# Performance work log

Measured on AMD Instinct MI355X. Metric: run time of the kernel, lower is better.

Reference implementation:

```python
import jax, jax.numpy as jnp
import numpy as np

TOP_K = 4
NORM_TOPK_PROB = True


def setup_inputs() -> dict:
    key = jax.random.key(0)
    kx, kg, k1, k3, k2 = jax.random.split(key, 5)
    B, S, H, I, E = 1, 2048, 1024, 512, 16
    scale = 0.02
    return {
        "hidden_states": jax.random.normal(kx, (B, S, H), jnp.float32),
        "gate_w": jax.random.normal(kg, (E, H), jnp.float32) * scale,   # router Linear weight [E,H]
        "w1": jax.random.normal(k1, (E, I, H), jnp.float32) * scale,    # intermediateDense per expert
        "w3": jax.random.normal(k3, (E, I, H), jnp.float32) * scale,    # intermediateDense2 per expert
        "w2": jax.random.normal(k2, (E, H, I), jnp.float32) * scale,    # outputDense per expert
    }


def reference(hidden_states, gate_w, w1, w3, w2):
    B, S, H = hidden_states.shape
    x = hidden_states.reshape(-1, H)                    # [T,H]
    T = x.shape[0]
    E = gate_w.shape[0]

    # Router: softmax in fp32, top-k, optional renorm (norm_topk_prob=True)
    router_logits = x @ gate_w.T                        # [T,E]
    probs = jax.nn.softmax(router_logits.astype(jnp.float32), axis=-1)
    routing_weights, selected = jax.lax.top_k(probs, TOP_K)   # [T,K], [T,K]
    if NORM_TOPK_PROB:
        routing_weights = routing_weights / routing_weights.sum(-1, keepdims=True)
    routing_weights = routing_weights.astype(x.dtype)

    # Dense per-token expert-weight matrix: zero for unselected experts, so
    # the combine below computes exactly the torch gather->FFN->index_add math.
    w = jnp.zeros((T, E), x.dtype).at[jnp.arange(T)[:, None], selected].add(routing_weights)

    # Gated SiLU FFN for every expert, combined with routing weights.
    h1 = jnp.einsum('th,eih->tei', x, w1)               # [T,E,I]
    h3 = jnp.einsum('th,eih->tei', x, w3)               # [T,E,I]
    act = jax.nn.silu(h1) * h3                          # [T,E,I]
    out = jnp.einsum('tei,ehi,te->th', act, w2, w)      # [T,H]
    return out.reshape(B, S, H)
```

## Files before the change

### kernel.cpp

```cpp
#include <hip/hip_runtime.h>
#include <hip/hip_bf16.h>

#define T 2048
#define H 1024
#define IDIM 512
#define E 16
#define TOPK 4
#define NPAIR (T * TOPK)

typedef short bf16x8 __attribute__((ext_vector_type(8)));
typedef float f32x4 __attribute__((ext_vector_type(4)));
typedef unsigned short u16x8 __attribute__((ext_vector_type(8)));

static __device__ __forceinline__ unsigned short f2bf(float f) {
    union { float f; unsigned int u; } v; v.f = f;
    unsigned int r = (v.u + 0x7FFFu + ((v.u >> 16) & 1u)) >> 16;
    return (unsigned short)r;
}
static __device__ __forceinline__ float bf2f(unsigned short s) {
    union { unsigned int u; float f; } v; v.u = ((unsigned int)s) << 16;
    return v.f;
}

static __device__ __forceinline__ void async_ld16(const unsigned short* g, unsigned short* l) {
    __builtin_amdgcn_global_load_lds((const __attribute__((address_space(1))) void*)g,
                                     (__attribute__((address_space(3))) void*)l, 16, 0, 0);
}

__global__ __launch_bounds__(256) void router_kernel(
    const float* __restrict__ x, const float* __restrict__ gw,
    int* __restrict__ topk_idx, float* __restrict__ topk_w,
    unsigned short* __restrict__ xb)
{
    int tok = blockIdx.x * 4 + (threadIdx.x >> 6);
    int lane = threadIdx.x & 63;
    if (tok >= T) return;
    const float4* xt4 = (const float4*)(x + (size_t)tok * H);
    float4 xr[4];
#pragma unroll
    for (int j = 0; j < 4; ++j) xr[j] = xt4[lane + j * 64];
    ushort4* xbt = (ushort4*)(xb + (size_t)tok * H);
#pragma unroll
    for (int j = 0; j < 4; ++j) {
        ushort4 o;
        o.x = f2bf(xr[j].x); o.y = f2bf(xr[j].y);
        o.z = f2bf(xr[j].z); o.w = f2bf(xr[j].w);
        xbt[lane + j * 64] = o;
    }
    float logits[E];
#pragma unroll
    for (int e = 0; e < E; ++e) {
        const float4* ge4 = (const float4*)(gw + (size_t)e * H);
        float acc = 0.f;
#pragma unroll
        for (int j = 0; j < 4; ++j) {
            float4 g = ge4[lane + j * 64];
            acc += xr[j].x * g.x + xr[j].y * g.y + xr[j].z * g.z + xr[j].w * g.w;
        }
#pragma unroll
        for (int off = 32; off; off >>= 1) acc += __shfl_xor(acc, off, 64);
        logits[e] = acc;
    }
    if (lane == 0) {
        float m = logits[0];
#pragma unroll
        for (int e = 1; e < E; ++e) m = fmaxf(m, logits[e]);
        float p[E];
#pragma unroll
        for (int e = 0; e < E; ++e) p[e] = __expf(logits[e] - m);
        int sel[TOPK]; float wv[TOPK]; float tot = 0.f;
#pragma unroll
        for (int k = 0; k < TOPK; ++k) {
            int best = 0; float bv = -1.f;
#pragma unroll
            for (int e = 0; e < E; ++e) { if (p[e] > bv) { bv = p[e]; best = e; } }
            sel[k] = best; wv[k] = bv; tot += bv; p[best] = -2.f;
        }
#pragma unroll
        for (int k = 0; k < TOPK; ++k) {
            topk_idx[tok * TOPK + k] = sel[k];
            topk_w[tok * TOPK + k] = wv[k] / tot;
        }
    }
}

__global__ __launch_bounds__(256) void cvtrb_kernel(
    const float* __restrict__ w1, const float* __restrict__ w3, const float* __restrict__ w2,
    unsigned short* __restrict__ d1, unsigned short* __restrict__ d3, unsigned short* __restrict__ d2,
    const int* __restrict__ topk_idx, int* __restrict__ offsets,
    int* __restrict__ pair_token, int* __restrict__ inv_pos)
{
    int tid = threadIdx.x;
    if (blockIdx.x == 0) {
        __shared__ int h[E];
        __shared__ int cur[E];
        if (tid < E) h[tid] = 0;
        __syncthreads();
        int eloc[32];
#pragma unroll
        for (int j = 0; j < 32; ++j) {
            eloc[j] = topk_idx[tid * 32 + j];
            atomicAdd(&h[eloc[j]], 1);
        }
        __syncthreads();
        if (tid == 0) {
            int s = 0;
#pragma unroll
            for (int e = 0; e < E; ++e) { offsets[e] = s; cur[e] = s; s += h[e]; }
            offsets[E] = s;
        }
        __syncthreads();
#pragma unroll
        for (int j = 0; j < 32; ++j) {
            int i = tid * 32 + j;
            int pos = atomicAdd(&cur[eloc[j]], 1);
            pair_token[pos] = i >> 2;
            inv_pos[i] = pos;
        }
        return;
    }
    const int n8 = (E * IDIM * H) / 8;
    int cb = blockIdx.x - 1;
    int region = cb >> 11;
    int bid = cb & 2047;
    const float* src = (region == 0) ? w1 : (region == 1) ? w3 : w2;
    unsigned short* dst = (region == 0) ? d1 : (region == 1) ? d3 : d2;
    int i = bid * 256 + tid;
    const int stride = 2048 * 256;
#pragma unroll 2
    for (; i < n8; i += stride) {
        float4 a = ((const float4*)src)[2 * i];
        float4 b = ((const float4*)src)[2 * i + 1];
        u16x8 o;
        o[0] = f2bf(a.x); o[1] = f2bf(a.y); o[2] = f2bf(a.z); o[3] = f2bf(a.w);
        o[4] = f2bf(b.x); o[5] = f2bf(b.y); o[6] = f2bf(b.z); o[7] = f2bf(b.w);
        ((u16x8*)dst)[i] = o;
    }
}


__global__ __launch_bounds__(256, 5) void gemm_a_kernel(
    const unsigned short* __restrict__ xb,
    const unsigned short* __restrict__ wb1,
    const unsigned short* __restrict__ wb3,
    const int* __restrict__ offsets,
    const int* __restrict__ pair_token,
    unsigned short* __restrict__ act)
{
    __shared__ unsigned short Xs[2][128 * 32];
    __shared__ unsigned short W1s[2][64 * 32];
    __shared__ unsigned short W3s[2][64 * 32];

    int bid = blockIdx.x;
    int xcd = bid & 7, s0 = bid >> 3;
    int yz = xcd * 16 + (s0 >> 4);
    int e = yz >> 3;
    int n0 = (yz & 7) * 64;
    int t0 = (s0 & 15) * 128;

    int beg = offsets[e];
    int cnt = offsets[e + 1] - beg;
    if (t0 >= cnt) return;

    int tid = threadIdx.x;
    int wave = tid >> 6, lane = tid & 63;

    const unsigned short* xg[2];
#pragma unroll
    for (int i = 0; i < 2; ++i) {
        int slot = wave * 128 + i * 64 + lane;
        int g = slot >> 3, sp = (slot & 7) ^ (g & 7);
        int row = g * 2 + (sp >> 2), c = sp & 3;
        int r = t0 + row; if (r >= cnt) r = cnt - 1;
        xg[i] = xb + (size_t)pair_token[beg + r] * H + c * 8;
    }
    const unsigned short* w1g;
    const unsigned short* w3g;
    {
        int slot = wave * 64 + lane;
        int g = slot >> 3, sp = (slot & 7) ^ (g & 7);
        int row = g * 2 + (sp >> 2), c = sp & 3;
        size_t off = (size_t)e * IDIM * H + (size_t)(n0 + row) * H + c * 8;
        w1g = wb1 + off;
        w3g = wb3 + off;
    }

    int wr = wave >> 1, wc = wave & 1;
    int lm = lane & 15, lq = lane >> 4;

    f32x4 acc1[4][2], acc3[4][2];
#pragma unroll
    for (int mi = 0; mi < 4; ++mi)
#pragma unroll
        for (int nj = 0; nj < 2; ++nj) {
            acc1[mi][nj] = (f32x4){0.f, 0.f, 0.f, 0.f};
            acc3[mi][nj] = (f32x4){0.f, 0.f, 0.f, 0.f};
        }

    int aoff[4], boff[2];
#pragma unroll
    for (int mi = 0; mi < 4; ++mi) {
        int m = wr * 64 + mi * 16 + lm;
        int g = m >> 1;
        aoff[mi] = g * 64 + (((lq + ((m & 1) << 2)) ^ (g & 7)) << 3);
    }
#pragma unroll
    for (int nj = 0; nj < 2; ++nj) {
        int n = wc * 32 + nj * 16 + lm;
        int g = n >> 1;
        boff[nj] = g * 64 + (((lq + ((n & 1) << 2)) ^ (g & 7)) << 3);
    }

#pragma unroll
    for (int i = 0; i < 2; ++i) async_ld16(xg[i], &Xs[0][(wave * 128 + i * 64) * 8]);
    async_ld16(w1g, &W1s[0][wave * 512]);
    async_ld16(w3g, &W3s[0][wave * 512]);

    const int NK = H / 32;
    for (int kk = 0; kk < NK; ++kk) {
        int cur = kk & 1;
        __syncthreads();
        if (kk + 1 < NK) {
            int nxt = cur ^ 1;
            int k1 = (kk + 1) * 32;
#pragma unroll
            for (int i = 0; i < 2; ++i) async_ld16(xg[i] + k1, &Xs[nxt][(wave * 128 + i * 64) * 8]);
            async_ld16(w1g + k1, &W1s[nxt][wave * 512]);
            async_ld16(w3g + k1, &W3s[nxt][wave * 512]);
        }
        bf16x8 af[4], b1[2], b3[2];
#pragma unroll
        for (int mi = 0; mi < 4; ++mi) af[mi] = *(const bf16x8*)&Xs[cur][aoff[mi]];
#pragma unroll
        for (int nj = 0; nj < 2; ++nj) {
            b1[nj] = *(const bf16x8*)&W1s[cur][boff[nj]];
            b3[nj] = *(const bf16x8*)&W3s[cur][boff[nj]];
        }
#pragma unroll
        for (int mi = 0; mi < 4; ++mi)
#pragma unroll
            for (int nj = 0; nj < 2; ++nj) {
                acc1[mi][nj] = __builtin_amdgcn_mfma_f32_16x16x32_bf16(af[mi], b1[nj], acc1[mi][nj], 0, 0, 0);
                acc3[mi][nj] = __builtin_amdgcn_mfma_f32_16x16x32_bf16(af[mi], b3[nj], acc3[mi][nj], 0, 0, 0);
            }
    }
#pragma unroll
    for (int mi = 0; mi < 4; ++mi) {
#pragma unroll
        for (int r = 0; r < 4; ++r) {
            int trow = t0 + wr * 64 + mi * 16 + lq * 4 + r;
            if (trow < cnt) {
                size_t base = (size_t)(beg + trow) * IDIM + n0 + wc * 32 + lm;
#pragma unroll
                for (int nj = 0; nj < 2; ++nj) {
                    float h1 = acc1[mi][nj][r];
                    float sg = h1 / (1.f + __expf(-h1));
                    act[base + nj * 16] = f2bf(sg * acc3[mi][nj][r]);
                }
            }
        }
    }
}

__global__ __launch_bounds__(256, 5) void gemm_b_kernel(
    const unsigned short* __restrict__ act,
    const unsigned short* __restrict__ wb2,
    const int* __restrict__ offsets,
    unsigned short* __restrict__ outp)
{
    __shared__ unsigned short As[2][128 * 32];
    __shared__ unsigned short W2s[2][64 * 32];

    int bid = blockIdx.x;
    int xcd = bid & 7, s0 = bid >> 3;
    int yz = xcd * 32 + (s0 >> 4);
    int e = yz >> 4;
    int h0 = (yz & 15) * 64;
    int t0 = (s0 & 15) * 128;

    int beg = offsets[e];
    int cnt = offsets[e + 1] - beg;
    if (t0 >= cnt) return;

    int tid = threadIdx.x;
    int wave = tid >> 6, lane = tid & 63;

    const unsigned short* ag[2];
#pragma unroll
    for (int i = 0; i < 2; ++i) {
        int slot = wave * 128 + i * 64 + lane;
        int g = slot >> 3, sp = (slot & 7) ^ (g & 7);
        int row = g * 2 + (sp >> 2), c = sp & 3;
        int ar = beg + t0 + row; if (ar > NPAIR - 1) ar = NPAIR - 1;
        ag[i] = act + (size_t)ar * IDIM + c * 8;
    }
    const unsigned short* w2g;
    {
        int slot = wave * 64 + lane;
        int g = slot >> 3, sp = (slot & 7) ^ (g & 7);
        int row = g * 2 + (sp >> 2), c = sp & 3;
        w2g = wb2 + (size_t)e * H * IDIM + (size_t)(h0 + row) * IDIM + c * 8;
    }

    int wr = wave >> 1, wc = wave & 1;
    int lm = lane & 15, lq = lane >> 4;

    f32x4 acc[4][2];
#pragma unroll
    for (int mi = 0; mi < 4; ++mi)
#pragma unroll
        for (int nj = 0; nj < 2; ++nj) acc[mi][nj] = (f32x4){0.f, 0.f, 0.f, 0.f};

    int aoff[4], boff[2];
#pragma unroll
    for (int mi = 0; mi < 4; ++mi) {
        int m = wr * 64 + mi * 16 + lm;
        int g = m >> 1;
        aoff[mi] = g * 64 + (((lq + ((m & 1) << 2)) ^ (g & 7)) << 3);
    }
#pragma unroll
    for (int nj = 0; nj < 2; ++nj) {
        int n = wc * 32 + nj * 16 + lm;
        int g = n >> 1;
        boff[nj] = g * 64 + (((lq + ((n & 1) << 2)) ^ (g & 7)) << 3);
    }

#pragma unroll
    for (int i = 0; i < 2; ++i) async_ld16(ag[i], &As[0][(wave * 128 + i * 64) * 8]);
    async_ld16(w2g, &W2s[0][wave * 512]);

    const int NK = IDIM / 32;
    for (int kk = 0; kk < NK; ++kk) {
        int cur = kk & 1;
        __syncthreads();
        if (kk + 1 < NK) {
            int nxt = cur ^ 1;
            int k1 = (kk + 1) * 32;
#pragma unroll
            for (int i = 0; i < 2; ++i) async_ld16(ag[i] + k1, &As[nxt][(wave * 128 + i * 64) * 8]);
            async_ld16(w2g + k1, &W2s[nxt][wave * 512]);
        }
        bf16x8 af[4], bfr[2];
#pragma unroll
        for (int mi = 0; mi < 4; ++mi) af[mi] = *(const bf16x8*)&As[cur][aoff[mi]];
#pragma unroll
        for (int nj = 0; nj < 2; ++nj) bfr[nj] = *(const bf16x8*)&W2s[cur][boff[nj]];
#pragma unroll
        for (int mi = 0; mi < 4; ++mi)
#pragma unroll
            for (int nj = 0; nj < 2; ++nj)
                acc[mi][nj] = __builtin_amdgcn_mfma_f32_16x16x32_bf16(af[mi], bfr[nj], acc[mi][nj], 0, 0, 0);
    }
#pragma unroll
    for (int mi = 0; mi < 4; ++mi) {
#pragma unroll
        for (int r = 0; r < 4; ++r) {
            int trow = t0 + wr * 64 + mi * 16 + lq * 4 + r;
            if (trow < cnt) {
                unsigned short* orow = outp + (size_t)(beg + trow) * H + h0 + wc * 32 + lm;
#pragma unroll
                for (int nj = 0; nj < 2; ++nj) orow[nj * 16] = f2bf(acc[mi][nj][r]);
            }
        }
    }
}

__global__ __launch_bounds__(256) void combine_kernel(
    const unsigned short* __restrict__ outp, const int* __restrict__ inv_pos,
    const float* __restrict__ topk_w, float* __restrict__ out)
{
    int gid = blockIdx.x * 256 + threadIdx.x;
    int t = gid >> 8;
    int c4 = gid & 255;
    float4 a = make_float4(0.f, 0.f, 0.f, 0.f);
#pragma unroll
    for (int k = 0; k < TOPK; ++k) {
        int pos = inv_pos[t * TOPK + k];
        float w = topk_w[t * TOPK + k];
        ushort4 v = ((const ushort4*)(outp + (size_t)pos * H))[c4];
        a.x += w * bf2f(v.x); a.y += w * bf2f(v.y);
        a.z += w * bf2f(v.z); a.w += w * bf2f(v.w);
    }
    *(float4*)(out + (size_t)t * H + c4 * 4) = a;
}

extern "C" void kernel_launch(void* const* d_in, const int* in_sizes, int n_in,
                              void* d_out, int out_size, void* d_ws, size_t ws_size,
                              hipStream_t stream)
{
    const float* x  = (const float*)d_in[0];
    const float* gw = (const float*)d_in[1];
    const float* w1 = (const float*)d_in[2];
    const float* w3 = (const float*)d_in[3];
    const float* w2 = (const float*)d_in[4];
    float* out = (float*)d_out;

    char* ws = (char*)d_ws;
    int*   offsets    = (int*)(ws + 128);
    int*   topk_idx   = (int*)(ws + 1024);
    float* topk_w     = (float*)(ws + 33792);
    int*   pair_token = (int*)(ws + 66560);
    int*   inv_pos    = (int*)(ws + 99328);
    unsigned short* xb  = (unsigned short*)(ws + 262144);
    unsigned short* wb1 = (unsigned short*)(ws + 8388608);
    unsigned short* wb3 = (unsigned short*)(ws + 25165824);
    unsigned short* wb2 = (unsigned short*)(ws + 41943040);
    unsigned short* act = (unsigned short*)(ws + 58720256);
    unsigned short* outp = (unsigned short*)(ws + 8388608);


    router_kernel<<<T / 4, 256, 0, stream>>>(x, gw, topk_idx, topk_w, xb);

    cvtrb_kernel<<<1 + 3 * 2048, 256, 0, stream>>>(
        w1, w3, w2, wb1, wb3, wb2, topk_idx, offsets, pair_token, inv_pos);

    gemm_a_kernel<<<2048, 256, 0, stream>>>(xb, wb1, wb3, offsets, pair_token, act);
    gemm_b_kernel<<<4096, 256, 0, stream>>>(act, wb2, offsets, outp);
    combine_kernel<<<(T * H / 4) / 256, 256, 0, stream>>>(outp, inv_pos, topk_w, out);
}
```

Measured before the change: 215.7 us.

## Overlap w2 bf16 conversion with the gate/up GEMM kernel

Moves the fp32-to-bf16 conversion of w2 out of the conversion kernel and into extra blocks appended to gemm_a_kernel. The w2 conversion is memory-bound and can then run alongside the compute-bound first expert GEMM instead of serialising before it. In exchange, the conversion blocks compete with GEMM blocks for bandwidth and CU slots, and gemm_a's launch_bounds/occupancy now covers a mixed workload.

```diff
diff --git a/kernel.cpp b/kernel.cpp
--- a/kernel.cpp
+++ b/kernel.cpp
@@ -85,8 +85,8 @@
 }
 
 __global__ __launch_bounds__(256) void cvtrb_kernel(
-    const float* __restrict__ w1, const float* __restrict__ w3, const float* __restrict__ w2,
-    unsigned short* __restrict__ d1, unsigned short* __restrict__ d3, unsigned short* __restrict__ d2,
+    const float* __restrict__ w1, const float* __restrict__ w3,
+    unsigned short* __restrict__ d1, unsigned short* __restrict__ d3,
     const int* __restrict__ topk_idx, int* __restrict__ offsets,
     int* __restrict__ pair_token, int* __restrict__ inv_pos)
 {
@@ -123,8 +123,8 @@
     int cb = blockIdx.x - 1;
     int region = cb >> 11;
     int bid = cb & 2047;
-    const float* src = (region == 0) ? w1 : (region == 1) ? w3 : w2;
-    unsigned short* dst = (region == 0) ? d1 : (region == 1) ? d3 : d2;
+    const float* src = (region == 0) ? w1 : w3;
+    unsigned short* dst = (region == 0) ? d1 : d3;
     int i = bid * 256 + tid;
     const int stride = 2048 * 256;
 #pragma unroll 2
@@ -143,10 +143,29 @@
     const unsigned short* __restrict__ xb,
     const unsigned short* __restrict__ wb1,
     const unsigned short* __restrict__ wb3,
+    const float* __restrict__ w2, unsigned short* __restrict__ wb2,
     const int* __restrict__ offsets,
     const int* __restrict__ pair_token,
     unsigned short* __restrict__ act)
 {
+    int tid = threadIdx.x;
+    if (blockIdx.x >= 2048) {
+        const int n8 = (E * H * IDIM) / 8;
+        int cb = blockIdx.x - 2048;
+        int i = cb * 256 + tid;
+        const int stride = 2048 * 256;
+#pragma unroll 2
+        for (; i < n8; i += stride) {
+            float4 a = ((const float4*)w2)[2 * i];
+            float4 b = ((const float4*)w2)[2 * i + 1];
+            u16x8 o;
+            o[0] = f2bf(a.x); o[1] = f2bf(a.y); o[2] = f2bf(a.z); o[3] = f2bf(a.w);
+            o[4] = f2bf(b.x); o[5] = f2bf(b.y); o[6] = f2bf(b.z); o[7] = f2bf(b.w);
+            ((u16x8*)wb2)[i] = o;
+        }
+        return;
+    }
+
     __shared__ unsigned short Xs[2][128 * 32];
     __shared__ unsigned short W1s[2][64 * 32];
     __shared__ unsigned short W3s[2][64 * 32];
@@ -162,7 +181,6 @@
     int cnt = offsets[e + 1] - beg;
     if (t0 >= cnt) return;
 
-    int tid = threadIdx.x;
     int wave = tid >> 6, lane = tid & 63;
 
     const unsigned short* xg[2];
@@ -408,13 +426,14 @@
     unsigned short* act = (unsigned short*)(ws + 58720256);
     unsigned short* outp = (unsigned short*)(ws + 8388608);
 
-
     router_kernel<<<T / 4, 256, 0, stream>>>(x, gw, topk_idx, topk_w, xb);
 
-    cvtrb_kernel<<<1 + 3 * 2048, 256, 0, stream>>>(
-        w1, w3, w2, wb1, wb3, wb2, topk_idx, offsets, pair_token, inv_pos);
-
-    gemm_a_kernel<<<2048, 256, 0, stream>>>(xb, wb1, wb3, offsets, pair_token, act);
+    cvtrb_kernel<<<1 + 2 * 2048, 256, 0, stream>>>(
+        w1, w3, wb1, wb3, topk_idx, offsets, pair_token, inv_pos);
+
+    gemm_a_kernel<<<2 * 2048, 256, 0, stream>>>(
+        xb, wb1, wb3, w2, wb2, offsets, pair_token, act);
+
     gemm_b_kernel<<<4096, 256, 0, stream>>>(act, wb2, offsets, outp);
     combine_kernel<<<(T * H / 4) / 256, 256, 0, stream>>>(outp, inv_pos, topk_w, out);
 }
```

After: 211.4 us. -2.0%, faster.

## Spread weight bf16 conversion across router and GEMM-A launches to overlap work

Applied to the files above, without the earlier changes.

The fp32-to-bf16 conversion of w1, w3 and w2 is split across three kernels. w1 is converted alongside the router, w3 alongside the routing/bucketing block, and w2 by extra blocks appended to the gate/up GEMM launch. The aim is to fill idle CUs during the small router and bucketing steps and overlap the w2 conversion with GEMM-A. The cost is that the extra blocks compete with GEMM-A for bandwidth and CU slots, and block scheduling order now decides how much real overlap occurs.

```diff
diff --git a/kernel.cpp b/kernel.cpp
--- a/kernel.cpp
+++ b/kernel.cpp
@@ -27,105 +27,11 @@
                                      (__attribute__((address_space(3))) void*)l, 16, 0, 0);
 }
 
-__global__ __launch_bounds__(256) void router_kernel(
-    const float* __restrict__ x, const float* __restrict__ gw,
-    int* __restrict__ topk_idx, float* __restrict__ topk_w,
-    unsigned short* __restrict__ xb)
-{
-    int tok = blockIdx.x * 4 + (threadIdx.x >> 6);
-    int lane = threadIdx.x & 63;
-    if (tok >= T) return;
-    const float4* xt4 = (const float4*)(x + (size_t)tok * H);
-    float4 xr[4];
-#pragma unroll
-    for (int j = 0; j < 4; ++j) xr[j] = xt4[lane + j * 64];
-    ushort4* xbt = (ushort4*)(xb + (size_t)tok * H);
-#pragma unroll
-    for (int j = 0; j < 4; ++j) {
-        ushort4 o;
-        o.x = f2bf(xr[j].x); o.y = f2bf(xr[j].y);
-        o.z = f2bf(xr[j].z); o.w = f2bf(xr[j].w);
-        xbt[lane + j * 64] = o;
-    }
-    float logits[E];
-#pragma unroll
-    for (int e = 0; e < E; ++e) {
-        const float4* ge4 = (const float4*)(gw + (size_t)e * H);
-        float acc = 0.f;
-#pragma unroll
-        for (int j = 0; j < 4; ++j) {
-            float4 g = ge4[lane + j * 64];
-            acc += xr[j].x * g.x + xr[j].y * g.y + xr[j].z * g.z + xr[j].w * g.w;
-        }
-#pragma unroll
-        for (int off = 32; off; off >>= 1) acc += __shfl_xor(acc, off, 64);
-        logits[e] = acc;
-    }
-    if (lane == 0) {
-        float m = logits[0];
-#pragma unroll
-        for (int e = 1; e < E; ++e) m = fmaxf(m, logits[e]);
-        float p[E];
-#pragma unroll
-        for (int e = 0; e < E; ++e) p[e] = __expf(logits[e] - m);
-        int sel[TOPK]; float wv[TOPK]; float tot = 0.f;
-#pragma unroll
-        for (int k = 0; k < TOPK; ++k) {
-            int best = 0; float bv = -1.f;
-#pragma unroll
-            for (int e = 0; e < E; ++e) { if (p[e] > bv) { bv = p[e]; best = e; } }
-            sel[k] = best; wv[k] = bv; tot += bv; p[best] = -2.f;
-        }
-#pragma unroll
-        for (int k = 0; k < TOPK; ++k) {
-            topk_idx[tok * TOPK + k] = sel[k];
-            topk_w[tok * TOPK + k] = wv[k] / tot;
-        }
-    }
-}
-
-__global__ __launch_bounds__(256) void cvtrb_kernel(
-    const float* __restrict__ w1, const float* __restrict__ w3, const float* __restrict__ w2,
-    unsigned short* __restrict__ d1, unsigned short* __restrict__ d3, unsigned short* __restrict__ d2,
-    const int* __restrict__ topk_idx, int* __restrict__ offsets,
-    int* __restrict__ pair_token, int* __restrict__ inv_pos)
-{
-    int tid = threadIdx.x;
-    if (blockIdx.x == 0) {
-        __shared__ int h[E];
-        __shared__ int cur[E];
-        if (tid < E) h[tid] = 0;
-        __syncthreads();
-        int eloc[32];
-#pragma unroll
-        for (int j = 0; j < 32; ++j) {
-            eloc[j] = topk_idx[tid * 32 + j];
-            atomicAdd(&h[eloc[j]], 1);
-        }
-        __syncthreads();
-        if (tid == 0) {
-            int s = 0;
-#pragma unroll
-            for (int e = 0; e < E; ++e) { offsets[e] = s; cur[e] = s; s += h[e]; }
-            offsets[E] = s;
-        }
-        __syncthreads();
-#pragma unroll
-        for (int j = 0; j < 32; ++j) {
-            int i = tid * 32 + j;
-            int pos = atomicAdd(&cur[eloc[j]], 1);
-            pair_token[pos] = i >> 2;
-            inv_pos[i] = pos;
-        }
-        return;
-    }
+static __device__ __forceinline__ void cvt_region(const float* __restrict__ src,
+                                                  unsigned short* __restrict__ dst,
+                                                  int cb, int tid) {
     const int n8 = (E * IDIM * H) / 8;
-    int cb = blockIdx.x - 1;
-    int region = cb >> 11;
-    int bid = cb & 2047;
-    const float* src = (region == 0) ? w1 : (region == 1) ? w3 : w2;
-    unsigned short* dst = (region == 0) ? d1 : (region == 1) ? d3 : d2;
-    int i = bid * 256 + tid;
+    int i = cb * 256 + tid;
     const int stride = 2048 * 256;
 #pragma unroll 2
     for (; i < n8; i += stride) {
@@ -138,15 +44,121 @@
     }
 }
 
+__global__ __launch_bounds__(256) void router_cvt1_kernel(
+    const float* __restrict__ x, const float* __restrict__ gw,
+    int* __restrict__ topk_idx, float* __restrict__ topk_w,
+    unsigned short* __restrict__ xb,
+    const float* __restrict__ w1, unsigned short* __restrict__ d1)
+{
+    int tid = threadIdx.x;
+    if (blockIdx.x >= 512) {
+        cvt_region(w1, d1, blockIdx.x - 512, tid);
+        return;
+    }
+    int tok = blockIdx.x * 4 + (tid >> 6);
+    int lane = tid & 63;
+    const float4* xt4 = (const float4*)(x + (size_t)tok * H);
+    float4 xr[4];
+#pragma unroll
+    for (int j = 0; j < 4; ++j) xr[j] = xt4[lane + j * 64];
+    ushort4* xbt = (ushort4*)(xb + (size_t)tok * H);
+#pragma unroll
+    for (int j = 0; j < 4; ++j) {
+        ushort4 o;
+        o.x = f2bf(xr[j].x); o.y = f2bf(xr[j].y);
+        o.z = f2bf(xr[j].z); o.w = f2bf(xr[j].w);
+        xbt[lane + j * 64] = o;
+    }
+    float logits[E];
+#pragma unroll
+    for (int e = 0; e < E; ++e) {
+        const float4* ge4 = (const float4*)(gw + (size_t)e * H);
+        float acc = 0.f;
+#pragma unroll
+        for (int j = 0; j < 4; ++j) {
+            float4 g = ge4[lane + j * 64];
+            acc += xr[j].x * g.x + xr[j].y * g.y + xr[j].z * g.z + xr[j].w * g.w;
+        }
+#pragma unroll
+        for (int off = 32; off; off >>= 1) acc += __shfl_xor(acc, off, 64);
+        logits[e] = acc;
+    }
+    if (lane == 0) {
+        float m = logits[0];
+#pragma unroll
+        for (int e = 1; e < E; ++e) m = fmaxf(m, logits[e]);
+        float p[E];
+#pragma unroll
+        for (int e = 0; e < E; ++e) p[e] = __expf(logits[e] - m);
+        int sel[TOPK]; float wv[TOPK]; float tot = 0.f;
+#pragma unroll
+        for (int k = 0; k < TOPK; ++k) {
+            int best = 0; float bv = -1.f;
+#pragma unroll
+            for (int e = 0; e < E; ++e) { if (p[e] > bv) { bv = p[e]; best = e; } }
+            sel[k] = best; wv[k] = bv; tot += bv; p[best] = -2.f;
+        }
+#pragma unroll
+        for (int k = 0; k < TOPK; ++k) {
+            topk_idx[tok * TOPK + k] = sel[k];
+            topk_w[tok * TOPK + k] = wv[k] / tot;
+        }
+    }
+}
+
+__global__ __launch_bounds__(256) void cvtrb_kernel(
+    const float* __restrict__ w3, unsigned short* __restrict__ d3,
+    const int* __restrict__ topk_idx, int* __restrict__ offsets,
+    int* __restrict__ pair_token, int* __restrict__ inv_pos)
+{
+    int tid = threadIdx.x;
+    if (blockIdx.x == 0) {
+        __shared__ int h[E];
+        __shared__ int cur[E];
+        if (tid < E) h[tid] = 0;
+        __syncthreads();
+        int eloc[32];
+#pragma unroll
+        for (int j = 0; j < 32; ++j) {
+            eloc[j] = topk_idx[tid * 32 + j];
+            atomicAdd(&h[eloc[j]], 1);
+        }
+        __syncthreads();
+        if (tid == 0) {
+            int s = 0;
+#pragma unroll
+            for (int e = 0; e < E; ++e) { offsets[e] = s; cur[e] = s; s += h[e]; }
+            offsets[E] = s;
+        }
+        __syncthreads();
+#pragma unroll
+        for (int j = 0; j < 32; ++j) {
+            int i = tid * 32 + j;
+            int pos = atomicAdd(&cur[eloc[j]], 1);
+            pair_token[pos] = i >> 2;
+            inv_pos[i] = pos;
+        }
+        return;
+    }
+    cvt_region(w3, d3, blockIdx.x - 1, tid);
+}
+
 
 __global__ __launch_bounds__(256, 5) void gemm_a_kernel(
     const unsigned short* __restrict__ xb,
     const unsigned short* __restrict__ wb1,
     const unsigned short* __restrict__ wb3,
+    const float* __restrict__ w2, unsigned short* __restrict__ wb2,
     const int* __restrict__ offsets,
     const int* __restrict__ pair_token,
     unsigned short* __restrict__ act)
 {
+    int tid = threadIdx.x;
+    if (blockIdx.x >= 2048) {
+        cvt_region(w2, wb2, blockIdx.x - 2048, tid);
+        return;
+    }
+
     __shared__ unsigned short Xs[2][128 * 32];
     __shared__ unsigned short W1s[2][64 * 32];
     __shared__ unsigned short W3s[2][64 * 32];
@@ -162,7 +174,6 @@
     int cnt = offsets[e + 1] - beg;
     if (t0 >= cnt) return;
 
-    int tid = threadIdx.x;
     int wave = tid >> 6, lane = tid & 63;
 
     const unsigned short* xg[2];
@@ -408,13 +419,15 @@
     unsigned short* act = (unsigned short*)(ws + 58720256);
     unsigned short* outp = (unsigned short*)(ws + 8388608);
 
-
-    router_kernel<<<T / 4, 256, 0, stream>>>(x, gw, topk_idx, topk_w, xb);
-
-    cvtrb_kernel<<<1 + 3 * 2048, 256, 0, stream>>>(
-        w1, w3, w2, wb1, wb3, wb2, topk_idx, offsets, pair_token, inv_pos);
-
-    gemm_a_kernel<<<2048, 256, 0, stream>>>(xb, wb1, wb3, offsets, pair_token, act);
+    router_cvt1_kernel<<<512 + 2048, 256, 0, stream>>>(
+        x, gw, topk_idx, topk_w, xb, w1, wb1);
+
+    cvtrb_kernel<<<1 + 2048, 256, 0, stream>>>(
+        w3, wb3, topk_idx, offsets, pair_token, inv_pos);
+
+    gemm_a_kernel<<<2 * 2048, 256, 0, stream>>>(
+        xb, wb1, wb3, w2, wb2, offsets, pair_token, act);
+
     gemm_b_kernel<<<4096, 256, 0, stream>>>(act, wb2, offsets, outp);
     combine_kernel<<<(T * H / 4) / 256, 256, 0, stream>>>(outp, inv_pos, topk_w, out);
 }
```

After: 212.4 us. No clear change (-1.5%).
